# Performance work log

Measured on AMD Instinct MI355X. Metric: run time of the kernel, lower is better.

## Reference

```python
import jax, jax.numpy as jnp
import numpy as np

B, C = 2, 2
D = H = W = 192
N_BIF = 64                 # bif ids 0..63; labels = bif*4 + stub (stub in 1..3)
NUM_LABELS = 4 * N_BIF     # 256
MIN_STUBS = 2
MIN_VOXELS = 1
TEMP = 0.2


def setup_inputs() -> dict:
    key = jax.random.key(0)
    k1, k2 = jax.random.split(key)
    pred = jax.random.normal(k1, (B, C, D, H, W), dtype=jnp.float32)
    stub_label_map = jax.random.randint(k2, (B, 1, D, H, W), 0, NUM_LABELS).astype(jnp.float32)
    return {"pred": pred, "stub_label_map": stub_label_map}


def reference(pred, stub_label_map):
    # foreground probability: softmax over channel dim, take class 1
    fg = jax.nn.softmax(pred, axis=1)[:, 1]                     # [B,D,H,W]
    labels = jnp.round(stub_label_map[:, 0]).astype(jnp.int32)  # [B,D,H,W]

    Bn = fg.shape[0]
    fg_flat = fg.reshape(Bn, -1)
    lab_flat = labels.reshape(Bn, -1)

    seg = lambda v, i: jax.ops.segment_sum(v, i, num_segments=NUM_LABELS)
    sums = jax.vmap(seg)(fg_flat, lab_flat)                      # [B, NUM_LABELS]
    counts = jax.vmap(seg)(jnp.ones_like(fg_flat), lab_flat)     # [B, NUM_LABELS]

    # group labels as [bif, stub]; drop bif 0 and stub 0 (never used in loop)
    sums = sums.reshape(Bn, N_BIF, 4)[:, 1:, 1:4]                # [B, N_BIF-1, 3]
    counts = counts.reshape(Bn, N_BIF, 4)[:, 1:, 1:4]

    valid = counts >= MIN_VOXELS                                 # stub has enough voxels
    means = sums / jnp.maximum(counts, 1.0)                      # per-stub mean fg prob

    # softmin over the valid stubs of each bif (masked softmax of -mean/temp)
    logits = jnp.where(valid, -means / TEMP, -1e9)
    weights = jax.nn.softmax(logits, axis=-1)
    score = jnp.sum(jnp.where(valid, means * weights, 0.0), axis=-1)  # [B, N_BIF-1]

    valid_bif = jnp.sum(valid, axis=-1) >= MIN_STUBS
    total = jnp.sum(jnp.where(valid_bif, 1.0 - score, 0.0))
    n_bifs = jnp.sum(valid_bif)
    return jnp.where(n_bifs > 0, total / jnp.maximum(n_bifs, 1).astype(total.dtype), 0.0)
```

## Files before the change

kernel.cpp:

```cpp
#include <hip/hip_runtime.h>
#include <math.h>

#define BATCH     2
#define NLAB      256
#define VOX       (192*192*192)
#define VVEC      (VOX/4)
#define TEMP      0.2f

#define STEP      4096.0f
#define INV_STEP  (1.0f/4096.0f)

__global__ __launch_bounds__(256) void histo_kernel(
    const float* __restrict__ pred,
    const float* __restrict__ labmap,
    float* __restrict__ ws_slots)
{
    __shared__ float s_hist[2 * NLAB];

    const int b = blockIdx.y;
    const int tid = threadIdx.x;

    s_hist[tid] = 0.0f;
    s_hist[tid + NLAB] = 0.0f;
    __syncthreads();

    const float4* p0 = (const float4*)(pred + (size_t)b * 2 * VOX);
    const float4* p1 = (const float4*)(pred + (size_t)b * 2 * VOX + VOX);
    const float4* lm = (const float4*)(labmap + (size_t)b * VOX);

    const int copy = (tid & 1) << 8;
    const int stride = gridDim.x * 256;
    for (int i = blockIdx.x * 256 + tid; i < VVEC; i += stride) {
        float4 a = p0[i];
        float4 c = p1[i];
        float4 l = lm[i];

        float fg0 = 1.0f / (1.0f + __expf(a.x - c.x));
        float fg1 = 1.0f / (1.0f + __expf(a.y - c.y));
        float fg2 = 1.0f / (1.0f + __expf(a.z - c.z));
        float fg3 = 1.0f / (1.0f + __expf(a.w - c.w));

        int l0 = ((int)(l.x + 0.5f)) & (NLAB - 1);
        int l1 = ((int)(l.y + 0.5f)) & (NLAB - 1);
        int l2 = ((int)(l.z + 0.5f)) & (NLAB - 1);
        int l3 = ((int)(l.w + 0.5f)) & (NLAB - 1);

        atomicAdd(&s_hist[copy + l0], STEP + fg0);
        atomicAdd(&s_hist[copy + l1], STEP + fg1);
        atomicAdd(&s_hist[copy + l2], STEP + fg2);
        atomicAdd(&s_hist[copy + l3], STEP + fg3);
    }
    __syncthreads();

    ws_slots[((size_t)(b * gridDim.x + blockIdx.x)) * NLAB + tid] =
        s_hist[tid] + s_hist[tid + NLAB];
}

__global__ __launch_bounds__(1024) void finalize_kernel(
    const float* __restrict__ ws_slots,
    int nslot,
    float* __restrict__ out)
{
    __shared__ float s_ps[BATCH][4][NLAB];
    __shared__ float s_pc[BATCH][4][NLAB];
    __shared__ float s_fsum[BATCH][NLAB];
    __shared__ float s_fcnt[BATCH][NLAB];

    const int tid  = threadIdx.x;
    const int bin  = tid & (NLAB - 1);
    const int part = tid >> 8;
    const int per  = (nslot + 3) >> 2;

    for (int b = 0; b < BATCH; ++b) {
        float cs = 0.0f, ss = 0.0f;
        int s0 = part * per;
        int s1 = s0 + per; if (s1 > nslot) s1 = nslot;
        for (int s = s0; s < s1; ++s) {
            float v = ws_slots[((size_t)(b * nslot + s)) * NLAB + bin];
            float c = floorf(v * INV_STEP);
            cs += c;
            ss += v - c * STEP;
        }
        s_ps[b][part][bin] = ss;
        s_pc[b][part][bin] = cs;
    }
    __syncthreads();

    if (tid < NLAB) {
        for (int b = 0; b < BATCH; ++b) {
            s_fsum[b][tid] = (s_ps[b][0][tid] + s_ps[b][1][tid])
                           + (s_ps[b][2][tid] + s_ps[b][3][tid]);
            s_fcnt[b][tid] = (s_pc[b][0][tid] + s_pc[b][1][tid])
                           + (s_pc[b][2][tid] + s_pc[b][3][tid]);
        }
    }
    __syncthreads();

    if (tid < 64) {
        float total = 0.0f;
        float nbifs = 0.0f;
        if (tid >= 1) {
            for (int bb = 0; bb < BATCH; ++bb) {
                float means[3];
                bool  valid[3];
                int   nvalid = 0;
                for (int s = 0; s < 3; ++s) {
                    int lab = tid * 4 + 1 + s;
                    float cnt = s_fcnt[bb][lab];
                    float sum = s_fsum[bb][lab];
                    valid[s] = (cnt >= 1.0f);
                    means[s] = sum / fmaxf(cnt, 1.0f);
                    nvalid  += valid[s] ? 1 : 0;
                }
                float logits[3], m = -3e38f;
                for (int s = 0; s < 3; ++s) {
                    logits[s] = valid[s] ? (-means[s] / TEMP) : -1e9f;
                    m = fmaxf(m, logits[s]);
                }
                float e[3], se = 0.0f;
                for (int s = 0; s < 3; ++s) { e[s] = __expf(logits[s] - m); se += e[s]; }
                float score = 0.0f;
                for (int s = 0; s < 3; ++s) {
                    if (valid[s]) score += means[s] * (e[s] / se);
                }
                if (nvalid >= 2) {
                    total += 1.0f - score;
                    nbifs += 1.0f;
                }
            }
        }
        for (int off = 32; off > 0; off >>= 1) {
            total += __shfl_down(total, off);
            nbifs += __shfl_down(nbifs, off);
        }
        if (tid == 0) {
            out[0] = (nbifs > 0.0f) ? (total / fmaxf(nbifs, 1.0f)) : 0.0f;
        }
    }
}

extern "C" void kernel_launch(void* const* d_in, const int* in_sizes, int n_in,
                              void* d_out, int out_size, void* d_ws, size_t ws_size,
                              hipStream_t stream) {
    const float* pred = (const float*)d_in[0];
    const float* lab  = (const float*)d_in[1];

    int gridx = 256;
    while ((size_t)gridx * BATCH * NLAB * sizeof(float) > ws_size && gridx > 8)
        gridx >>= 1;

    dim3 grid(gridx, BATCH);
    histo_kernel<<<grid, 256, 0, stream>>>(pred, lab, (float*)d_ws);
    finalize_kernel<<<1, 1024, 0, stream>>>((const float*)d_ws, gridx,
                                            (float*)d_out);
}
```

Measured before the change: 246.2 us.

## Split histogram atomics between LDS and global copies, double grid width

Iterations of the voxel loop now alternate between shared-memory atomics and float atomics into 64 zero-initialised global histogram copies per batch. The grid is also fixed at 512 blocks instead of 256. The aim is to spread atomic traffic across LDS and L2, since the kernel is bound by atomic throughput rather than memory bandwidth. The finalize kernel merges both sets and rounds the packed counts to nearest. In exchange it adds a memset and heavy L2 atomic contention, drops the workspace-size check, and loses precision in the global copies, which accumulate much larger packed values.

```diff
diff --git a/kernel.cpp b/kernel.cpp
--- a/kernel.cpp
+++ b/kernel.cpp
@@ -6,6 +6,8 @@
 #define VOX       (192*192*192)
 #define VVEC      (VOX/4)
 #define TEMP      0.2f
+#define GRIDX     512
+#define NCOPY     64
 
 #define STEP      4096.0f
 #define INV_STEP  (1.0f/4096.0f)
@@ -13,7 +15,8 @@
 __global__ __launch_bounds__(256) void histo_kernel(
     const float* __restrict__ pred,
     const float* __restrict__ labmap,
-    float* __restrict__ ws_slots)
+    float* __restrict__ ws_slots,
+    float* __restrict__ gcopies)
 {
     __shared__ float s_hist[2 * NLAB];
 
@@ -29,8 +32,12 @@
     const float4* lm = (const float4*)(labmap + (size_t)b * VOX);
 
     const int copy = (tid & 1) << 8;
-    const int stride = gridDim.x * 256;
-    for (int i = blockIdx.x * 256 + tid; i < VVEC; i += stride) {
+    float* gbase = gcopies +
+        ((size_t)b * NCOPY + ((blockIdx.x * 4 + (tid >> 6)) & (NCOPY - 1))) * NLAB;
+
+    const int stride = GRIDX * 256;
+    int it = 0;
+    for (int i = blockIdx.x * 256 + tid; i < VVEC; i += stride, ++it) {
         float4 a = p0[i];
         float4 c = p1[i];
         float4 l = lm[i];
@@ -45,20 +52,27 @@
         int l2 = ((int)(l.z + 0.5f)) & (NLAB - 1);
         int l3 = ((int)(l.w + 0.5f)) & (NLAB - 1);
 
-        atomicAdd(&s_hist[copy + l0], STEP + fg0);
-        atomicAdd(&s_hist[copy + l1], STEP + fg1);
-        atomicAdd(&s_hist[copy + l2], STEP + fg2);
-        atomicAdd(&s_hist[copy + l3], STEP + fg3);
+        if (it & 1) {
+            atomicAdd(&gbase[l0], STEP + fg0);
+            atomicAdd(&gbase[l1], STEP + fg1);
+            atomicAdd(&gbase[l2], STEP + fg2);
+            atomicAdd(&gbase[l3], STEP + fg3);
+        } else {
+            atomicAdd(&s_hist[copy + l0], STEP + fg0);
+            atomicAdd(&s_hist[copy + l1], STEP + fg1);
+            atomicAdd(&s_hist[copy + l2], STEP + fg2);
+            atomicAdd(&s_hist[copy + l3], STEP + fg3);
+        }
     }
     __syncthreads();
 
-    ws_slots[((size_t)(b * gridDim.x + blockIdx.x)) * NLAB + tid] =
+    ws_slots[((size_t)(b * GRIDX + blockIdx.x)) * NLAB + tid] =
         s_hist[tid] + s_hist[tid + NLAB];
 }
 
 __global__ __launch_bounds__(1024) void finalize_kernel(
     const float* __restrict__ ws_slots,
-    int nslot,
+    const float* __restrict__ gcopies,
     float* __restrict__ out)
 {
     __shared__ float s_ps[BATCH][4][NLAB];
@@ -69,15 +83,20 @@
     const int tid  = threadIdx.x;
     const int bin  = tid & (NLAB - 1);
     const int part = tid >> 8;
-    const int per  = (nslot + 3) >> 2;
+    const int perS = GRIDX / 4;
+    const int perC = NCOPY / 4;
 
     for (int b = 0; b < BATCH; ++b) {
         float cs = 0.0f, ss = 0.0f;
-        int s0 = part * per;
-        int s1 = s0 + per; if (s1 > nslot) s1 = nslot;
-        for (int s = s0; s < s1; ++s) {
-            float v = ws_slots[((size_t)(b * nslot + s)) * NLAB + bin];
-            float c = floorf(v * INV_STEP);
+        for (int s = part * perS; s < (part + 1) * perS; ++s) {
+            float v = ws_slots[((size_t)(b * GRIDX + s)) * NLAB + bin];
+            float c = floorf(v * INV_STEP + 0.5f);
+            cs += c;
+            ss += v - c * STEP;
+        }
+        for (int s = part * perC; s < (part + 1) * perC; ++s) {
+            float v = gcopies[((size_t)(b * NCOPY + s)) * NLAB + bin];
+            float c = floorf(v * INV_STEP + 0.5f);
             cs += c;
             ss += v - c * STEP;
         }
@@ -145,12 +164,13 @@
     const float* pred = (const float*)d_in[0];
     const float* lab  = (const float*)d_in[1];
 
-    int gridx = 256;
-    while ((size_t)gridx * BATCH * NLAB * sizeof(float) > ws_size && gridx > 8)
-        gridx >>= 1;
+    float* ws_slots = (float*)d_ws;
+    float* gcopies  = ws_slots + (size_t)BATCH * GRIDX * NLAB;
 
-    dim3 grid(gridx, BATCH);
-    histo_kernel<<<grid, 256, 0, stream>>>(pred, lab, (float*)d_ws);
-    finalize_kernel<<<1, 1024, 0, stream>>>((const float*)d_ws, gridx,
-                                            (float*)d_out);
+    hipMemsetAsync(gcopies, 0, (size_t)BATCH * NCOPY * NLAB * sizeof(float),
+                   stream);
+
+    dim3 grid(GRIDX, BATCH);
+    histo_kernel<<<grid, 256, 0, stream>>>(pred, lab, ws_slots, gcopies);
+    finalize_kernel<<<1, 1024, 0, stream>>>(ws_slots, gcopies, (float*)d_out);
 }
```

Measured after the change: 351.4 us. 1.43x slower.
